# Kernel tuning notes

Hardware: AMD Instinct MI355X
Metric: run time of the kernel (lower is better)

The kernel has to match this reference:

```python
import jax, jax.numpy as jnp
import numpy as np

N = 100000
E = 1600000
F_IN = 32
HID = 16
C_OUT = 10
K = 4


def setup_inputs() -> dict:
    key = jax.random.key(0)
    k1, k2, k3, k4, k5, k6, k7 = jax.random.split(key, 7)
    x = jax.random.normal(k1, (N, F_IN), dtype=jnp.float32)
    edge_index = jax.random.randint(k2, (2, E), 0, N, dtype=jnp.int64)
    # ChebConv weights: one [in, out] matrix per Chebyshev order k
    W1 = jax.random.normal(k3, (K, F_IN, HID), dtype=jnp.float32) / np.sqrt(F_IN)
    b1 = jax.random.normal(k4, (HID,), dtype=jnp.float32) * 0.01
    W2 = jax.random.normal(k5, (K, HID, C_OUT), dtype=jnp.float32) / np.sqrt(HID)
    b2 = jax.random.normal(k6, (C_OUT,), dtype=jnp.float32) * 0.01
    return {"x": x, "edge_index": edge_index, "W1": W1, "b1": b1, "W2": W2, "b2": b2}


def _cheb_conv(h, src, dst, norm, W, b, num_nodes):
    # Tx_0 = h; Tx_1 = L_hat h; Tx_k = 2 L_hat Tx_{k-1} - Tx_{k-2}
    def prop(v):  # v: [N, F] -> L_hat v via sparse gather/scatter
        return jax.ops.segment_sum(norm[:, None] * v[src], dst, num_segments=num_nodes)

    Tx0 = h
    out = Tx0 @ W[0]
    Tx1 = prop(h)
    out = out + Tx1 @ W[1]
    for k in range(2, W.shape[0]):
        Tx2 = 2.0 * prop(Tx1) - Tx0
        out = out + Tx2 @ W[k]
        Tx0, Tx1 = Tx1, Tx2
    return out + b


def reference(x, edge_index, W1, b1, W2, b2):
    src, dst = edge_index[0], edge_index[1]
    num_nodes = x.shape[0]
    # symmetric normalization with lambda_max = 2: L_hat = -D^{-1/2} A D^{-1/2}
    deg = jax.ops.segment_sum(jnp.ones((src.shape[0],), dtype=x.dtype), dst, num_segments=num_nodes)
    dis = jnp.where(deg > 0, jax.lax.rsqrt(jnp.maximum(deg, 1.0)), 0.0)
    norm = -dis[src] * dis[dst]
    h = _cheb_conv(x, src, dst, norm, W1, b1, num_nodes)
    h = jax.nn.relu(h)
    # dropout is identity in eval mode
    h = _cheb_conv(h, src, dst, norm, W2, b2, num_nodes)
    return jax.nn.log_softmax(h, axis=1)
```

## Files before the change

kernel.cpp:

```cpp
#include <hip/hip_runtime.h>
#include <hip/hip_bf16.h>
#include <math.h>


#define BLK 256
#define BLKP 512
#define NBUCK_MAX 256
#define CHUNK 4096
#define CAPB 16384
#define PLACE_CAP 10240

__device__ inline unsigned short f32_to_bf16_rne(float f) {
    unsigned int u = __float_as_uint(f);
    unsigned int rounding = 0x7FFFu + ((u >> 16) & 1u);
    return (unsigned short)((u + rounding) >> 16);
}
__device__ inline unsigned int pack_bf16x2(float a, float b) {
    return (unsigned int)f32_to_bf16_rne(a) | ((unsigned int)f32_to_bf16_rne(b) << 16);
}
__device__ inline void unpack8(const uint4 u, float* f) {
    const unsigned int* p = &u.x;
#pragma unroll
    for (int j = 0; j < 4; j++) {
        unsigned int w = p[j];
        f[2 * j]     = __uint_as_float(w << 16);
        f[2 * j + 1] = __uint_as_float(w & 0xFFFF0000u);
    }
}
__device__ inline void add8(const uint4 u, float* acc) {
    const unsigned int* p = &u.x;
#pragma unroll
    for (int j = 0; j < 4; j++) {
        unsigned int w = p[j];
        acc[2 * j]     += __uint_as_float(w << 16);
        acc[2 * j + 1] += __uint_as_float(w & 0xFFFF0000u);
    }
}
__device__ inline uint4 pack8(const float* r) {
    uint4 o;
    o.x = pack_bf16x2(r[0], r[1]);
    o.y = pack_bf16x2(r[2], r[3]);
    o.z = pack_bf16x2(r[4], r[5]);
    o.w = pack_bf16x2(r[6], r[7]);
    return o;
}

__device__ inline void gather_sum(const int* __restrict__ psrc, int b, int e,
                                  const uint4* __restrict__ vb, int c, float* acc) {
    int i = b;
    for (; i + 7 < e; i += 8) {
        int s0 = psrc[i],     s1 = psrc[i + 1], s2 = psrc[i + 2], s3 = psrc[i + 3];
        int s4 = psrc[i + 4], s5 = psrc[i + 5], s6 = psrc[i + 6], s7 = psrc[i + 7];
        uint4 a0 = vb[(size_t)s0 * 2 + c];
        uint4 a1 = vb[(size_t)s1 * 2 + c];
        uint4 a2 = vb[(size_t)s2 * 2 + c];
        uint4 a3 = vb[(size_t)s3 * 2 + c];
        uint4 a4 = vb[(size_t)s4 * 2 + c];
        uint4 a5 = vb[(size_t)s5 * 2 + c];
        uint4 a6 = vb[(size_t)s6 * 2 + c];
        uint4 a7 = vb[(size_t)s7 * 2 + c];
        add8(a0, acc); add8(a1, acc); add8(a2, acc); add8(a3, acc);
        add8(a4, acc); add8(a5, acc); add8(a6, acc); add8(a7, acc);
    }
    for (; i + 3 < e; i += 4) {
        int s0 = psrc[i], s1 = psrc[i + 1], s2 = psrc[i + 2], s3 = psrc[i + 3];
        uint4 a0 = vb[(size_t)s0 * 2 + c];
        uint4 a1 = vb[(size_t)s1 * 2 + c];
        uint4 a2 = vb[(size_t)s2 * 2 + c];
        uint4 a3 = vb[(size_t)s3 * 2 + c];
        add8(a0, acc); add8(a1, acc); add8(a2, acc); add8(a3, acc);
    }
    for (; i < e; i++) add8(vb[(size_t)psrc[i] * 2 + c], acc);
}

__global__ __launch_bounds__(BLK)
void binned_scatter_kernel(const int* __restrict__ src, const int* __restrict__ dst,
                           int* __restrict__ bfill, int* __restrict__ tmp,
                           int E, int nbuck) {
    __shared__ int cnt[NBUCK_MAX];
    __shared__ int lofs[NBUCK_MAX + 1];
    __shared__ int pos[NBUCK_MAX];
    __shared__ int gbase[NBUCK_MAX];
    __shared__ int stage[CHUNK];
    __shared__ unsigned char bkt[CHUNK];

    int tid = threadIdx.x;
    int e0 = blockIdx.x * CHUNK;
    int nE = min(CHUNK, E - e0);

    for (int b = tid; b < nbuck; b += BLK) { cnt[b] = 0; pos[b] = 0; }
    __syncthreads();

    for (int i = tid; i < nE; i += BLK) {
        int d = dst[e0 + i];
        atomicAdd(&cnt[d >> 9], 1);
    }
    __syncthreads();

    {
        int v = (tid < nbuck) ? cnt[tid] : 0;
        lofs[tid] = v;
        __syncthreads();
        for (int off = 1; off < BLK; off <<= 1) {
            int t = (tid >= off) ? lofs[tid - off] : 0;
            __syncthreads();
            lofs[tid] += t;
            __syncthreads();
        }
        int incl = lofs[tid];
        __syncthreads();
        lofs[tid] = incl - v;
        if (tid == 0) lofs[nbuck] = nE;
        if (tid < nbuck && v > 0)
            gbase[tid] = tid * CAPB + atomicAdd(&bfill[tid], v);
    }
    __syncthreads();

    for (int i = tid; i < nE; i += BLK) {
        int s = src[e0 + i];
        int d = dst[e0 + i];
        int b = d >> 9;
        int slot = lofs[b] + atomicAdd(&pos[b], 1);
        stage[slot] = (s << 9) | (d & 511);
        bkt[slot] = (unsigned char)b;
    }
    __syncthreads();

    for (int i = tid; i < nE; i += BLK) {
        int b = bkt[i];
        tmp[gbase[b] + (i - lofs[b])] = stage[i];
    }
}

__global__ __launch_bounds__(BLKP)
void bucket_place_kernel(const int* __restrict__ bfill, const int* __restrict__ tmp,
                         int* __restrict__ psrc, int2* __restrict__ rows,
                         float* __restrict__ dis, float* __restrict__ d2,
                         float* __restrict__ inv, int N) {
    __shared__ int cnt[512];
    __shared__ int ofs[512];
    __shared__ int fill[512];
    __shared__ int stage[PLACE_CAP];

    int b = blockIdx.x;
    int tid = threadIdx.x;
    int n0 = b << 9;
    int nn = min(512, N - n0);
    int S = b * CAPB;
    int tot = bfill[b];

    cnt[tid] = 0;
    fill[tid] = 0;
    __syncthreads();

    for (int i = tid; i < tot; i += BLKP)
        atomicAdd(&cnt[tmp[S + i] & 511], 1);
    __syncthreads();

    int v = cnt[tid];
    ofs[tid] = v;
    __syncthreads();
    for (int off = 1; off < BLKP; off <<= 1) {
        int t = (tid >= off) ? ofs[tid - off] : 0;
        __syncthreads();
        ofs[tid] += t;
        __syncthreads();
    }
    int excl = ofs[tid] - v;
    __syncthreads();
    ofs[tid] = excl;
    if (tid < nn) {
        int n = n0 + tid;
        rows[n] = make_int2(S + excl, S + excl + v);
        float fv = (float)v;
        dis[n] = (v > 0) ? rsqrtf(fv) : 0.0f;
        d2[n]  = (v > 0) ? 1.0f / fv : 0.0f;
        inv[n] = (v > 0) ? sqrtf(fv) : 0.0f;
    }
    __syncthreads();

    if (tot <= PLACE_CAP) {
        for (int i = tid; i < tot; i += BLKP) {
            int rec = tmp[S + i];
            int nl = rec & 511;
            int slot = ofs[nl] + atomicAdd(&fill[nl], 1);
            stage[slot] = rec >> 9;
        }
        __syncthreads();
        for (int i = tid; i < tot; i += BLKP) psrc[S + i] = stage[i];
    } else {
        for (int i = tid; i < tot; i += BLKP) {
            int rec = tmp[S + i];
            int nl = rec & 511;
            int slot = S + ofs[nl] + atomicAdd(&fill[nl], 1);
            psrc[slot] = rec >> 9;
        }
    }
}


__global__ __launch_bounds__(BLK)
void zgen_kernel(const float* __restrict__ x, const float* __restrict__ dis,
                 const float* __restrict__ W1,
                 uint4* __restrict__ z0t, uint4* __restrict__ uz1t,
                 uint4* __restrict__ uz2t, uint4* __restrict__ uz3t,
                 uint4* __restrict__ z2rt, int N) {
    __shared__ float sW[4 * 32 * 16];
    for (int i = threadIdx.x; i < 4 * 32 * 16; i += blockDim.x) sW[i] = W1[i];
    __syncthreads();
    int t = blockIdx.x * blockDim.x + threadIdx.x;
    int n = t >> 1;
    int h = t & 1;
    if (n >= N) return;
    float acc0[8], acc1[8], acc2[8], acc3[8];
#pragma unroll
    for (int j = 0; j < 8; j++) { acc0[j] = 0.f; acc1[j] = 0.f; acc2[j] = 0.f; acc3[j] = 0.f; }
    const float4* x4 = reinterpret_cast<const float4*>(x + (size_t)n * 32);
#pragma unroll
    for (int q = 0; q < 8; q++) {
        float4 a = x4[q];
        float xi[4] = {a.x, a.y, a.z, a.w};
#pragma unroll
        for (int u = 0; u < 4; u++) {
            const float* Wb = sW + (q * 4 + u) * 16 + h * 8;
            float xv = xi[u];
#pragma unroll
            for (int j = 0; j < 8; j++) {
                acc0[j] += xv * Wb[j];
                acc1[j] += xv * Wb[512 + j];
                acc2[j] += xv * Wb[1024 + j];
                acc3[j] += xv * Wb[1536 + j];
            }
        }
    }
    float dn = dis[n];
    float s1[8], s2[8], s3[8];
#pragma unroll
    for (int j = 0; j < 8; j++) { s1[j] = dn * acc1[j]; s2[j] = dn * acc2[j]; s3[j] = dn * acc3[j]; }
    size_t o = (size_t)n * 2 + h;
    z0t[o]  = pack8(acc0);
    uz1t[o] = pack8(s1);
    uz2t[o] = pack8(s2);
    z2rt[o] = pack8(acc2);
    uz3t[o] = pack8(s3);
}

template <bool HAVE_SUB>
__global__ __launch_bounds__(BLK)
void prop_cl_kernel(const int2* __restrict__ rows,
                    const int* __restrict__ psrc, const float* __restrict__ d2,
                    const uint4* __restrict__ vb, const uint4* __restrict__ addt,
                    const uint4* __restrict__ subt, uint4* __restrict__ outb, int N) {
    int t = blockIdx.x * blockDim.x + threadIdx.x;
    int n = t >> 2;
    int l = t & 3;
    int c = l & 1;
    int hf = l >> 1;
    if (n >= N) return;
    int2 rw = rows[n];
    int beg = rw.x;
    int end = rw.y;
    int mid = beg + ((end - beg) >> 1);
    int b = hf ? mid : beg;
    int e = hf ? end : mid;
    float acc[8];
#pragma unroll
    for (int j = 0; j < 8; j++) acc[j] = 0.f;
    gather_sum(psrc, b, e, vb, c, acc);
#pragma unroll
    for (int j = 0; j < 8; j++) acc[j] += __shfl_xor(acc[j], 2);
    if (hf) return;
    float f = -2.0f * d2[n];
    float ad[8], r[8];
    unpack8(addt[(size_t)n * 2 + c], ad);
    if (HAVE_SUB) {
        float sb[8];
        unpack8(subt[(size_t)n * 2 + c], sb);
#pragma unroll
        for (int j = 0; j < 8; j++) r[j] = f * acc[j] + ad[j] - sb[j];
    } else {
#pragma unroll
        for (int j = 0; j < 8; j++) r[j] = f * acc[j] + ad[j];
    }
    outb[(size_t)n * 2 + c] = pack8(r);
}

__global__ __launch_bounds__(BLK)
void final1_kernel(const int2* __restrict__ rows,
                   const int* __restrict__ psrc, const float* __restrict__ dis,
                   const float* __restrict__ d2, const float* __restrict__ inv,
                   const uint4* __restrict__ ub1t, const uint4* __restrict__ ub2t,
                   const uint4* __restrict__ z0t, const uint4* __restrict__ z2rt,
                   const float* __restrict__ W2, const float* __restrict__ b1,
                   uint4* __restrict__ w0t, uint4* __restrict__ uw1t,
                   uint4* __restrict__ uw2t, uint4* __restrict__ uw3t,
                   uint4* __restrict__ w2rt, int N) {
    __shared__ float sW[4 * 16 * 16];
    __shared__ float sb1[16];
    for (int i = threadIdx.x; i < 4 * 16 * 16; i += blockDim.x) {
        int k = i >> 8, rem = i & 255, j = rem >> 4, o = rem & 15;
        sW[i] = (o < 10) ? W2[k * 160 + j * 10 + o] : 0.0f;
    }
    if (threadIdx.x < 16) sb1[threadIdx.x] = b1[threadIdx.x];
    __syncthreads();
    int t = blockIdx.x * blockDim.x + threadIdx.x;
    int n = t >> 1;
    int h = t & 1;
    if (n >= N) return;
    int2 rw = rows[n];
    float acc[8];
#pragma unroll
    for (int j = 0; j < 8; j++) acc[j] = 0.f;
    gather_sum(psrc, rw.x, rw.y, ub1t, h, acc);
    size_t o2 = (size_t)n * 2 + h;
    float z0[8], hrow[8];
    unpack8(z0t[o2], z0);
    if (d2[n] == 0.0f) {
        float z2[8];
        unpack8(z2rt[o2], z2);
#pragma unroll
        for (int j = 0; j < 8; j++) hrow[j] = fmaxf(sb1[h * 8 + j] + z0[j] - z2[j], 0.0f);
    } else {
        float b2v[8];
        unpack8(ub2t[o2], b2v);
        float dn = dis[n], iv = inv[n];
#pragma unroll
        for (int j = 0; j < 8; j++)
            hrow[j] = fmaxf(sb1[h * 8 + j] + z0[j] - dn * acc[j] - iv * b2v[j], 0.0f);
    }
    float h16[16];
#pragma unroll
    for (int j = 0; j < 8; j++) {
        float other = __shfl_xor(hrow[j], 1);
        h16[h * 8 + j] = hrow[j];
        h16[(1 - h) * 8 + j] = other;
    }
    float w0[8], w1[8], w2[8], w3[8];
#pragma unroll
    for (int o = 0; o < 8; o++) { w0[o] = 0.f; w1[o] = 0.f; w2[o] = 0.f; w3[o] = 0.f; }
#pragma unroll
    for (int j = 0; j < 16; j++) {
        float hv = h16[j];
        const float* Wb = sW + j * 16 + h * 8;
#pragma unroll
        for (int o = 0; o < 8; o++) {
            w0[o] += hv * Wb[o];
            w1[o] += hv * Wb[256 + o];
            w2[o] += hv * Wb[512 + o];
            w3[o] += hv * Wb[768 + o];
        }
    }
    float dn = dis[n];
    float s1[8], s2[8], s3[8];
#pragma unroll
    for (int o = 0; o < 8; o++) { s1[o] = dn * w1[o]; s2[o] = dn * w2[o]; s3[o] = dn * w3[o]; }
    w0t[o2]  = pack8(w0);
    uw1t[o2] = pack8(s1);
    uw2t[o2] = pack8(s2);
    w2rt[o2] = pack8(w2);
    uw3t[o2] = pack8(s3);
}

__global__ __launch_bounds__(BLK)
void final2_kernel(const int2* __restrict__ rows,
                   const int* __restrict__ psrc, const float* __restrict__ dis,
                   const float* __restrict__ d2, const float* __restrict__ inv,
                   const uint4* __restrict__ uv1t, const uint4* __restrict__ uv2t,
                   const uint4* __restrict__ w0t, const uint4* __restrict__ w2rt,
                   const float* __restrict__ b2, float* __restrict__ out, int N) {
    __shared__ float sb2[16];
    if (threadIdx.x < 16) sb2[threadIdx.x] = (threadIdx.x < 10) ? b2[threadIdx.x] : 0.0f;
    __syncthreads();
    int t = blockIdx.x * blockDim.x + threadIdx.x;
    int n = t >> 2;
    int l = t & 3;
    int c = l & 1;
    int hf = l >> 1;
    if (n >= N) return;
    int2 rw = rows[n];
    int beg = rw.x;
    int end = rw.y;
    int mid = beg + ((end - beg) >> 1);
    int gb = hf ? mid : beg;
    int ge = hf ? end : mid;
    float acc[8];
#pragma unroll
    for (int j = 0; j < 8; j++) acc[j] = 0.f;
    gather_sum(psrc, gb, ge, uv1t, c, acc);
#pragma unroll
    for (int j = 0; j < 8; j++) acc[j] += __shfl_xor(acc[j], 2);
    if (hf) return;
    size_t o2 = (size_t)n * 2 + c;
    float w0[8], L[8];
    unpack8(w0t[o2], w0);
    if (d2[n] == 0.0f) {
        float w2[8];
        unpack8(w2rt[o2], w2);
#pragma unroll
        for (int j = 0; j < 8; j++) L[j] = sb2[c * 8 + j] + w0[j] - w2[j];
    } else {
        float v2[8];
        unpack8(uv2t[o2], v2);
        float dn = dis[n], iv = inv[n];
#pragma unroll
        for (int j = 0; j < 8; j++)
            L[j] = sb2[c * 8 + j] + w0[j] - dn * acc[j] - iv * v2[j];
    }
    int nreal = (c == 0) ? 8 : 2;
    float m = -3.0e38f;
    for (int j = 0; j < nreal; j++) m = fmaxf(m, L[j]);
    m = fmaxf(m, __shfl_xor(m, 1));
    float s = 0.0f;
    for (int j = 0; j < nreal; j++) s += expf(L[j] - m);
    s += __shfl_xor(s, 1);
    float lse = m + logf(s);
    float* op = out + (size_t)n * 10 + c * 8;
    for (int j = 0; j < nreal; j++) op[j] = L[j] - lse;
}

extern "C" void kernel_launch(void* const* d_in, const int* in_sizes, int n_in,
                              void* d_out, int out_size, void* d_ws, size_t ws_size,
                              hipStream_t stream) {
    const float* x  = (const float*)d_in[0];
    const int*   ei = (const int*)d_in[1];
    const float* W1 = (const float*)d_in[2];
    const float* b1 = (const float*)d_in[3];
    const float* W2 = (const float*)d_in[4];
    const float* b2 = (const float*)d_in[5];
    float* out = (float*)d_out;

    const int N = in_sizes[0] / 32;
    const int E = in_sizes[1] / 2;
    const int* src = ei;
    const int* dst = ei + E;

    const int nbuck = (N + 511) / 512;

    char* w = (char*)d_ws;
    int*   bfill  = (int*)w;              w += NBUCK_MAX * 4;
    int2*  rows   = (int2*)w;             w += (size_t)(N + 8) * 8;
    float* dis    = (float*)w;            w += (size_t)N * 4;
    float* d2     = (float*)w;            w += (size_t)N * 4;
    float* inv    = (float*)w;            w += (size_t)N * 4;
    int*   tmp    = (int*)w;              w += (size_t)NBUCK_MAX * CAPB * 4;
    int*   psrc   = (int*)w;              w += (size_t)NBUCK_MAX * CAPB * 4;
    uint4* z0t    = (uint4*)w;            w += (size_t)32 * N;
    uint4* uz1t   = (uint4*)w;            w += (size_t)32 * N;
    uint4* uz2t   = (uint4*)w;            w += (size_t)32 * N;
    uint4* uz3t   = (uint4*)w;            w += (size_t)32 * N;
    uint4* z2rt   = (uint4*)w;            w += (size_t)32 * N;
    uint4* ub2t   = (uint4*)w;            w += (size_t)32 * N;
    uint4* ub1t   = (uint4*)w;            w += (size_t)32 * N;
    uint4* w0t    = (uint4*)w;            w += (size_t)32 * N;
    uint4* uw1t   = (uint4*)w;            w += (size_t)32 * N;
    uint4* uw2t   = (uint4*)w;            w += (size_t)32 * N;
    uint4* uw3t   = (uint4*)w;            w += (size_t)32 * N;
    uint4* w2rt   = (uint4*)w;            w += (size_t)32 * N;
    uint4* uv2t   = (uint4*)w;            w += (size_t)32 * N;
    uint4* uv1t   = (uint4*)w;            w += (size_t)32 * N;

    int gN2 = (N * 2 + BLK - 1) / BLK;
    int gN4 = (N * 4 + BLK - 1) / BLK;
    int gCH = (E + CHUNK - 1) / CHUNK;

    hipMemsetAsync(bfill, 0, NBUCK_MAX * sizeof(int), stream);
    binned_scatter_kernel<<<gCH, BLK, 0, stream>>>(src, dst, bfill, tmp, E, nbuck);
    bucket_place_kernel<<<nbuck, BLKP, 0, stream>>>(bfill, tmp, psrc, rows,
                                                    dis, d2, inv, N);

    zgen_kernel<<<gN2, BLK, 0, stream>>>(x, dis, W1, z0t, uz1t, uz2t, uz3t, z2rt, N);
    prop_cl_kernel<false><<<gN4, BLK, 0, stream>>>(rows, psrc, d2,
                                                   uz3t, uz2t, nullptr, ub2t, N);
    prop_cl_kernel<true ><<<gN4, BLK, 0, stream>>>(rows, psrc, d2,
                                                   ub2t, uz1t, uz3t, ub1t, N);
    final1_kernel<<<gN2, BLK, 0, stream>>>(rows, psrc, dis, d2, inv,
                                           ub1t, ub2t, z0t, z2rt, W2, b1,
                                           w0t, uw1t, uw2t, uw3t, w2rt, N);

    prop_cl_kernel<false><<<gN4, BLK, 0, stream>>>(rows, psrc, d2,
                                                   uw3t, uw2t, nullptr, uv2t, N);
    prop_cl_kernel<true ><<<gN4, BLK, 0, stream>>>(rows, psrc, d2,
                                                   uv2t, uw1t, uw3t, uv1t, N);
    final2_kernel<<<gN4, BLK, 0, stream>>>(rows, psrc, dis, d2, inv,
                                           uv1t, uv2t, w0t, w2rt, b2, out, N);
}
```

Measured before the change: 242.8 us.

## Compute node degrees during binning and use wave-shuffle scans in CSR build

The binning kernel now keeps each thread's 16 destination indices in registers and reuses them across passes. It also atomically accumulates per-node degrees into a global array, so the placement kernel no longer re-reads the bucket to count per-node entries. Both block-level prefix scans move from shared-memory Hillis-Steele loops with many barriers to 64-lane wave shuffle scans plus a small cross-wave sum. This trades a second pass over tmp for about 1.6M global atomics on the degree array and a larger memset.

New measurement: 296.3 us. 22.0% more time.

```diff
diff --git a/kernel.cpp b/kernel.cpp
--- a/kernel.cpp
+++ b/kernel.cpp
@@ -7,6 +7,7 @@
 #define BLKP 512
 #define NBUCK_MAX 256
 #define CHUNK 4096
+#define EPT 16
 #define CAPB 16384
 #define PLACE_CAP 10240
 
@@ -75,12 +76,13 @@
 
 __global__ __launch_bounds__(BLK)
 void binned_scatter_kernel(const int* __restrict__ src, const int* __restrict__ dst,
-                           int* __restrict__ bfill, int* __restrict__ tmp,
-                           int E, int nbuck) {
+                           int* __restrict__ bfill, int* __restrict__ deg,
+                           int* __restrict__ tmp, int E, int nbuck) {
     __shared__ int cnt[NBUCK_MAX];
-    __shared__ int lofs[NBUCK_MAX + 1];
+    __shared__ int lofs[NBUCK_MAX];
     __shared__ int pos[NBUCK_MAX];
     __shared__ int gbase[NBUCK_MAX];
+    __shared__ int wsum[4];
     __shared__ int stage[CHUNK];
     __shared__ unsigned char bkt[CHUNK];
 
@@ -91,38 +93,52 @@
     for (int b = tid; b < nbuck; b += BLK) { cnt[b] = 0; pos[b] = 0; }
     __syncthreads();
 
-    for (int i = tid; i < nE; i += BLK) {
-        int d = dst[e0 + i];
-        atomicAdd(&cnt[d >> 9], 1);
+    int myd[EPT];
+#pragma unroll
+    for (int k = 0; k < EPT; k++) {
+        int i = tid + k * BLK;
+        myd[k] = (i < nE) ? dst[e0 + i] : -1;
+    }
+#pragma unroll
+    for (int k = 0; k < EPT; k++) {
+        if (myd[k] >= 0) {
+            atomicAdd(&cnt[myd[k] >> 9], 1);
+            atomicAdd(&deg[myd[k]], 1);
+        }
     }
     __syncthreads();
 
     {
         int v = (tid < nbuck) ? cnt[tid] : 0;
-        lofs[tid] = v;
+        int lane = tid & 63, wv = tid >> 6;
+        int x = v;
+#pragma unroll
+        for (int off = 1; off < 64; off <<= 1) {
+            int y = __shfl_up(x, off);
+            if (lane >= off) x += y;
+        }
+        if (lane == 63) wsum[wv] = x;
         __syncthreads();
-        for (int off = 1; off < BLK; off <<= 1) {
-            int t = (tid >= off) ? lofs[tid - off] : 0;
-            __syncthreads();
-            lofs[tid] += t;
-            __syncthreads();
-        }
-        int incl = lofs[tid];
-        __syncthreads();
-        lofs[tid] = incl - v;
-        if (tid == 0) lofs[nbuck] = nE;
-        if (tid < nbuck && v > 0)
-            gbase[tid] = tid * CAPB + atomicAdd(&bfill[tid], v);
-    }
-    __syncthreads();
-
-    for (int i = tid; i < nE; i += BLK) {
-        int s = src[e0 + i];
-        int d = dst[e0 + i];
-        int b = d >> 9;
-        int slot = lofs[b] + atomicAdd(&pos[b], 1);
-        stage[slot] = (s << 9) | (d & 511);
-        bkt[slot] = (unsigned char)b;
+        int wo = 0;
+        for (int k = 0; k < wv; k++) wo += wsum[k];
+        int excl = x + wo - v;
+        if (tid < nbuck) {
+            lofs[tid] = excl;
+            if (v > 0) gbase[tid] = tid * CAPB + atomicAdd(&bfill[tid], v);
+        }
+    }
+    __syncthreads();
+
+#pragma unroll
+    for (int k = 0; k < EPT; k++) {
+        int i = tid + k * BLK;
+        if (myd[k] >= 0) {
+            int s = src[e0 + i];
+            int b = myd[k] >> 9;
+            int slot = lofs[b] + atomicAdd(&pos[b], 1);
+            stage[slot] = (s << 9) | (myd[k] & 511);
+            bkt[slot] = (unsigned char)b;
+        }
     }
     __syncthreads();
 
@@ -133,13 +149,14 @@
 }
 
 __global__ __launch_bounds__(BLKP)
-void bucket_place_kernel(const int* __restrict__ bfill, const int* __restrict__ tmp,
+void bucket_place_kernel(const int* __restrict__ bfill, const int* __restrict__ deg,
+                         const int* __restrict__ tmp,
                          int* __restrict__ psrc, int2* __restrict__ rows,
                          float* __restrict__ dis, float* __restrict__ d2,
                          float* __restrict__ inv, int N) {
-    __shared__ int cnt[512];
     __shared__ int ofs[512];
     __shared__ int fill[512];
+    __shared__ int wsum[8];
     __shared__ int stage[PLACE_CAP];
 
     int b = blockIdx.x;
@@ -149,25 +166,21 @@
     int S = b * CAPB;
     int tot = bfill[b];
 
-    cnt[tid] = 0;
+    int v = (tid < nn) ? deg[n0 + tid] : 0;
     fill[tid] = 0;
-    __syncthreads();
-
-    for (int i = tid; i < tot; i += BLKP)
-        atomicAdd(&cnt[tmp[S + i] & 511], 1);
-    __syncthreads();
-
-    int v = cnt[tid];
-    ofs[tid] = v;
-    __syncthreads();
-    for (int off = 1; off < BLKP; off <<= 1) {
-        int t = (tid >= off) ? ofs[tid - off] : 0;
-        __syncthreads();
-        ofs[tid] += t;
-        __syncthreads();
-    }
-    int excl = ofs[tid] - v;
-    __syncthreads();
+
+    int lane = tid & 63, wv = tid >> 6;
+    int x = v;
+#pragma unroll
+    for (int off = 1; off < 64; off <<= 1) {
+        int y = __shfl_up(x, off);
+        if (lane >= off) x += y;
+    }
+    if (lane == 63) wsum[wv] = x;
+    __syncthreads();
+    int wo = 0;
+    for (int k = 0; k < wv; k++) wo += wsum[k];
+    int excl = x + wo - v;
     ofs[tid] = excl;
     if (tid < nn) {
         int n = n0 + tid;
@@ -438,6 +451,7 @@
 
     char* w = (char*)d_ws;
     int*   bfill  = (int*)w;              w += NBUCK_MAX * 4;
+    int*   deg    = (int*)w;              w += (size_t)(N + 16) * 4;
     int2*  rows   = (int2*)w;             w += (size_t)(N + 8) * 8;
     float* dis    = (float*)w;            w += (size_t)N * 4;
     float* d2     = (float*)w;            w += (size_t)N * 4;
@@ -463,9 +477,9 @@
     int gN4 = (N * 4 + BLK - 1) / BLK;
     int gCH = (E + CHUNK - 1) / CHUNK;
 
-    hipMemsetAsync(bfill, 0, NBUCK_MAX * sizeof(int), stream);
-    binned_scatter_kernel<<<gCH, BLK, 0, stream>>>(src, dst, bfill, tmp, E, nbuck);
-    bucket_place_kernel<<<nbuck, BLKP, 0, stream>>>(bfill, tmp, psrc, rows,
+    hipMemsetAsync(bfill, 0, (NBUCK_MAX + N + 16) * sizeof(int), stream);
+    binned_scatter_kernel<<<gCH, BLK, 0, stream>>>(src, dst, bfill, deg, tmp, E, nbuck);
+    bucket_place_kernel<<<nbuck, BLKP, 0, stream>>>(bfill, deg, tmp, psrc, rows,
                                                     dis, d2, inv, N);
 
     zgen_kernel<<<gN2, BLK, 0, stream>>>(x, dis, W1, z0t, uz1t, uz2t, uz3t, z2rt, N);
```

## Store layer-2 features as 10-wide split bf16 arrays to cut gather bytes

Applied to the files above, without the earlier changes.

Layer-2 intermediates were padded to 16 bf16 channels (32 bytes per node). They are now split into a 16-byte uint4 array holding channels 0-7 and a 4-byte array holding channels 8-9, so each gathered edge reads 20 bytes instead of 32. A new prop_l2_kernel and the reworked final2_kernel use one thread pair per node covering all 10 channels, with the edge list split in half and reduced by a shuffle. The log-softmax no longer needs a cross-lane reduction. The cost is two separate loads per edge, one of them a narrow 4-byte scattered load, and fewer threads per node.

New measurement: 249.9 us. 1.03x slower.

```diff
diff --git a/kernel.cpp b/kernel.cpp
--- a/kernel.cpp
+++ b/kernel.cpp
@@ -27,6 +27,10 @@
         f[2 * j + 1] = __uint_as_float(w & 0xFFFF0000u);
     }
 }
+__device__ inline void unpack2(unsigned int w, float* f) {
+    f[0] = __uint_as_float(w << 16);
+    f[1] = __uint_as_float(w & 0xFFFF0000u);
+}
 __device__ inline void add8(const uint4 u, float* acc) {
     const unsigned int* p = &u.x;
 #pragma unroll
@@ -35,6 +39,10 @@
         acc[2 * j]     += __uint_as_float(w << 16);
         acc[2 * j + 1] += __uint_as_float(w & 0xFFFF0000u);
     }
+}
+__device__ inline void add2(unsigned int w, float* acc) {
+    acc[0] += __uint_as_float(w << 16);
+    acc[1] += __uint_as_float(w & 0xFFFF0000u);
 }
 __device__ inline uint4 pack8(const float* r) {
     uint4 o;
@@ -71,6 +79,36 @@
         add8(a0, acc); add8(a1, acc); add8(a2, acc); add8(a3, acc);
     }
     for (; i < e; i++) add8(vb[(size_t)psrc[i] * 2 + c], acc);
+}
+
+__device__ inline void gather_sum10(const int* __restrict__ psrc, int b, int e,
+                                    const uint4* __restrict__ vA,
+                                    const unsigned int* __restrict__ vB, float* acc) {
+    int i = b;
+    for (; i + 7 < e; i += 8) {
+        int s0 = psrc[i],     s1 = psrc[i + 1], s2 = psrc[i + 2], s3 = psrc[i + 3];
+        int s4 = psrc[i + 4], s5 = psrc[i + 5], s6 = psrc[i + 6], s7 = psrc[i + 7];
+        uint4 a0 = vA[s0], a1 = vA[s1], a2 = vA[s2], a3 = vA[s3];
+        uint4 a4 = vA[s4], a5 = vA[s5], a6 = vA[s6], a7 = vA[s7];
+        unsigned int q0 = vB[s0], q1 = vB[s1], q2 = vB[s2], q3 = vB[s3];
+        unsigned int q4 = vB[s4], q5 = vB[s5], q6 = vB[s6], q7 = vB[s7];
+        add8(a0, acc); add8(a1, acc); add8(a2, acc); add8(a3, acc);
+        add8(a4, acc); add8(a5, acc); add8(a6, acc); add8(a7, acc);
+        add2(q0, acc + 8); add2(q1, acc + 8); add2(q2, acc + 8); add2(q3, acc + 8);
+        add2(q4, acc + 8); add2(q5, acc + 8); add2(q6, acc + 8); add2(q7, acc + 8);
+    }
+    for (; i + 3 < e; i += 4) {
+        int s0 = psrc[i], s1 = psrc[i + 1], s2 = psrc[i + 2], s3 = psrc[i + 3];
+        uint4 a0 = vA[s0], a1 = vA[s1], a2 = vA[s2], a3 = vA[s3];
+        unsigned int q0 = vB[s0], q1 = vB[s1], q2 = vB[s2], q3 = vB[s3];
+        add8(a0, acc); add8(a1, acc); add8(a2, acc); add8(a3, acc);
+        add2(q0, acc + 8); add2(q1, acc + 8); add2(q2, acc + 8); add2(q3, acc + 8);
+    }
+    for (; i < e; i++) {
+        int s = psrc[i];
+        add8(vA[s], acc);
+        add2(vB[s], acc + 8);
+    }
 }
 
 __global__ __launch_bounds__(BLK)
@@ -292,9 +330,11 @@
                    const uint4* __restrict__ ub1t, const uint4* __restrict__ ub2t,
                    const uint4* __restrict__ z0t, const uint4* __restrict__ z2rt,
                    const float* __restrict__ W2, const float* __restrict__ b1,
-                   uint4* __restrict__ w0t, uint4* __restrict__ uw1t,
-                   uint4* __restrict__ uw2t, uint4* __restrict__ uw3t,
-                   uint4* __restrict__ w2rt, int N) {
+                   uint4* __restrict__ w0A, unsigned int* __restrict__ w0B,
+                   uint4* __restrict__ uw1A, unsigned int* __restrict__ uw1B,
+                   uint4* __restrict__ uw2A, unsigned int* __restrict__ uw2B,
+                   uint4* __restrict__ uw3A, unsigned int* __restrict__ uw3B,
+                   uint4* __restrict__ w2rA, unsigned int* __restrict__ w2rB, int N) {
     __shared__ float sW[4 * 16 * 16];
     __shared__ float sb1[16];
     for (int i = threadIdx.x; i < 4 * 16 * 16; i += blockDim.x) {
@@ -354,28 +394,79 @@
     float s1[8], s2[8], s3[8];
 #pragma unroll
     for (int o = 0; o < 8; o++) { s1[o] = dn * w1[o]; s2[o] = dn * w2[o]; s3[o] = dn * w3[o]; }
-    w0t[o2]  = pack8(w0);
-    uw1t[o2] = pack8(s1);
-    uw2t[o2] = pack8(s2);
-    w2rt[o2] = pack8(w2);
-    uw3t[o2] = pack8(s3);
+    if (h == 0) {
+        w0A[n]  = pack8(w0);
+        uw1A[n] = pack8(s1);
+        uw2A[n] = pack8(s2);
+        w2rA[n] = pack8(w2);
+        uw3A[n] = pack8(s3);
+    } else {
+        w0B[n]  = pack_bf16x2(w0[0], w0[1]);
+        uw1B[n] = pack_bf16x2(s1[0], s1[1]);
+        uw2B[n] = pack_bf16x2(s2[0], s2[1]);
+        w2rB[n] = pack_bf16x2(w2[0], w2[1]);
+        uw3B[n] = pack_bf16x2(s3[0], s3[1]);
+    }
+}
+
+template <bool HAVE_SUB>
+__global__ __launch_bounds__(BLK)
+void prop_l2_kernel(const int2* __restrict__ rows,
+                    const int* __restrict__ psrc, const float* __restrict__ d2,
+                    const uint4* __restrict__ vA, const unsigned int* __restrict__ vB,
+                    const uint4* __restrict__ addA, const unsigned int* __restrict__ addB,
+                    const uint4* __restrict__ subA, const unsigned int* __restrict__ subB,
+                    uint4* __restrict__ outA, unsigned int* __restrict__ outB, int N) {
+    int t = blockIdx.x * blockDim.x + threadIdx.x;
+    int n = t >> 1;
+    int hf = t & 1;
+    if (n >= N) return;
+    int2 rw = rows[n];
+    int beg = rw.x;
+    int end = rw.y;
+    int mid = beg + ((end - beg) >> 1);
+    int b = hf ? mid : beg;
+    int e = hf ? end : mid;
+    float acc[10];
+#pragma unroll
+    for (int j = 0; j < 10; j++) acc[j] = 0.f;
+    gather_sum10(psrc, b, e, vA, vB, acc);
+#pragma unroll
+    for (int j = 0; j < 10; j++) acc[j] += __shfl_xor(acc[j], 1);
+    if (hf) return;
+    float f = -2.0f * d2[n];
+    float ad[10], r[10];
+    unpack8(addA[n], ad);
+    unpack2(addB[n], ad + 8);
+    if (HAVE_SUB) {
+        float sb[10];
+        unpack8(subA[n], sb);
+        unpack2(subB[n], sb + 8);
+#pragma unroll
+        for (int j = 0; j < 10; j++) r[j] = f * acc[j] + ad[j] - sb[j];
+    } else {
+#pragma unroll
+        for (int j = 0; j < 10; j++) r[j] = f * acc[j] + ad[j];
+    }
+    outA[n] = pack8(r);
+    outB[n] = pack_bf16x2(r[8], r[9]);
 }
 
 __global__ __launch_bounds__(BLK)
 void final2_kernel(const int2* __restrict__ rows,
                    const int* __restrict__ psrc, const float* __restrict__ dis,
                    const float* __restrict__ d2, const float* __restrict__ inv,
-                   const uint4* __restrict__ uv1t, const uint4* __restrict__ uv2t,
-                   const uint4* __restrict__ w0t, const uint4* __restrict__ w2rt,
+                   const uint4* __restrict__ uv1A, const unsigned int* __restrict__ uv1B,
+                   const uint4* __restrict__ uv2A, const unsigned int* __restrict__ uv2B,
+                   const uint4* __restrict__ w0A, const unsigned int* __restrict__ w0B,
+                   const uint4* __restrict__ w2rA, const unsigned int* __restrict__ w2rB,
                    const float* __restrict__ b2, float* __restrict__ out, int N) {
     __shared__ float sb2[16];
     if (threadIdx.x < 16) sb2[threadIdx.x] = (threadIdx.x < 10) ? b2[threadIdx.x] : 0.0f;
     __syncthreads();
     int t = blockIdx.x * blockDim.x + threadIdx.x;
-    int n = t >> 2;
-    int l = t & 3;
-    int c = l & 1;
-    int hf = l >> 1;
+    int n = t >> 1;
+    int hf = t & 1;
     if (n >= N) return;
     int2 rw = rows[n];
     int beg = rw.x;
@@ -383,39 +474,41 @@
     int mid = beg + ((end - beg) >> 1);
     int gb = hf ? mid : beg;
     int ge = hf ? end : mid;
-    float acc[8];
-#pragma unroll
-    for (int j = 0; j < 8; j++) acc[j] = 0.f;
-    gather_sum(psrc, gb, ge, uv1t, c, acc);
-#pragma unroll
-    for (int j = 0; j < 8; j++) acc[j] += __shfl_xor(acc[j], 2);
+    float acc[10];
+#pragma unroll
+    for (int j = 0; j < 10; j++) acc[j] = 0.f;
+    gather_sum10(psrc, gb, ge, uv1A, uv1B, acc);
+#pragma unroll
+    for (int j = 0; j < 10; j++) acc[j] += __shfl_xor(acc[j], 1);
     if (hf) return;
-    size_t o2 = (size_t)n * 2 + c;
-    float w0[8], L[8];
-    unpack8(w0t[o2], w0);
+    float w0[10], L[10];
+    unpack8(w0A[n], w0);
+    unpack2(w0B[n], w0 + 8);
     if (d2[n] == 0.0f) {
-        float w2[8];
-        unpack8(w2rt[o2], w2);
-#pragma unroll
-        for (int j = 0; j < 8; j++) L[j] = sb2[c * 8 + j] + w0[j] - w2[j];
+        float w2[10];
+        unpack8(w2rA[n], w2);
+        unpack2(w2rB[n], w2 + 8);
+#pragma unroll
+        for (int j = 0; j < 10; j++) L[j] = sb2[j] + w0[j] - w2[j];
     } else {
-        float v2[8];
-        unpack8(uv2t[o2], v2);
+        float v2[10];
+        unpack8(uv2A[n], v2);
+        unpack2(uv2B[n], v2 + 8);
         float dn = dis[n], iv = inv[n];
 #pragma unroll
-        for (int j = 0; j < 8; j++)
-            L[j] = sb2[c * 8 + j] + w0[j] - dn * acc[j] - iv * v2[j];
-    }
-    int nreal = (c == 0) ? 8 : 2;
-    float m = -3.0e38f;
-    for (int j = 0; j < nreal; j++) m = fmaxf(m, L[j]);
-    m = fmaxf(m, __shfl_xor(m, 1));
+        for (int j = 0; j < 10; j++)
+            L[j] = sb2[j] + w0[j] - dn * acc[j] - iv * v2[j];
+    }
+    float m = L[0];
+#pragma unroll
+    for (int j = 1; j < 10; j++) m = fmaxf(m, L[j]);
     float s = 0.0f;
-    for (int j = 0; j < nreal; j++) s += expf(L[j] - m);
-    s += __shfl_xor(s, 1);
+#pragma unroll
+    for (int j = 0; j < 10; j++) s += expf(L[j] - m);
     float lse = m + logf(s);
-    float* op = out + (size_t)n * 10 + c * 8;
-    for (int j = 0; j < nreal; j++) op[j] = L[j] - lse;
+    float* op = out + (size_t)n * 10;
+#pragma unroll
+    for (int j = 0; j < 10; j++) op[j] = L[j] - lse;
 }
 
 extern "C" void kernel_launch(void* const* d_in, const int* in_sizes, int n_in,
@@ -451,13 +544,20 @@
     uint4* z2rt   = (uint4*)w;            w += (size_t)32 * N;
     uint4* ub2t   = (uint4*)w;            w += (size_t)32 * N;
     uint4* ub1t   = (uint4*)w;            w += (size_t)32 * N;
-    uint4* w0t    = (uint4*)w;            w += (size_t)32 * N;
-    uint4* uw1t   = (uint4*)w;            w += (size_t)32 * N;
-    uint4* uw2t   = (uint4*)w;            w += (size_t)32 * N;
-    uint4* uw3t   = (uint4*)w;            w += (size_t)32 * N;
-    uint4* w2rt   = (uint4*)w;            w += (size_t)32 * N;
-    uint4* uv2t   = (uint4*)w;            w += (size_t)32 * N;
-    uint4* uv1t   = (uint4*)w;            w += (size_t)32 * N;
+    uint4* w0A    = (uint4*)w;            w += (size_t)16 * N;
+    uint4* uw1A   = (uint4*)w;            w += (size_t)16 * N;
+    uint4* uw2A   = (uint4*)w;            w += (size_t)16 * N;
+    uint4* uw3A   = (uint4*)w;            w += (size_t)16 * N;
+    uint4* w2rA   = (uint4*)w;            w += (size_t)16 * N;
+    uint4* uv2A   = (uint4*)w;            w += (size_t)16 * N;
+    uint4* uv1A   = (uint4*)w;            w += (size_t)16 * N;
+    unsigned int* w0B  = (unsigned int*)w; w += (size_t)4 * N;
+    unsigned int* uw1B = (unsigned int*)w; w += (size_t)4 * N;
+    unsigned int* uw2B = (unsigned int*)w; w += (size_t)4 * N;
+    unsigned int* uw3B = (unsigned int*)w; w += (size_t)4 * N;
+    unsigned int* w2rB = (unsigned int*)w; w += (size_t)4 * N;
+    unsigned int* uv2B = (unsigned int*)w; w += (size_t)4 * N;
+    unsigned int* uv1B = (unsigned int*)w; w += (size_t)4 * N;
 
     int gN2 = (N * 2 + BLK - 1) / BLK;
     int gN4 = (N * 4 + BLK - 1) / BLK;
@@ -475,12 +575,16 @@
                                                    ub2t, uz1t, uz3t, ub1t, N);
     final1_kernel<<<gN2, BLK, 0, stream>>>(rows, psrc, dis, d2, inv,
                                            ub1t, ub2t, z0t, z2rt, W2, b1,
-                                           w0t, uw1t, uw2t, uw3t, w2rt, N);
-
-    prop_cl_kernel<false><<<gN4, BLK, 0, stream>>>(rows, psrc, d2,
-                                                   uw3t, uw2t, nullptr, uv2t, N);
-    prop_cl_kernel<true ><<<gN4, BLK, 0, stream>>>(rows, psrc, d2,
-                                                   uv2t, uw1t, uw3t, uv1t, N);
-    final2_kernel<<<gN4, BLK, 0, stream>>>(rows, psrc, dis, d2, inv,
-                                           uv1t, uv2t, w0t, w2rt, b2, out, N);
-}
+                                           w0A, w0B, uw1A, uw1B, uw2A, uw2B,
+                                           uw3A, uw3B, w2rA, w2rB, N);
+
+    prop_l2_kernel<false><<<gN2, BLK, 0, stream>>>(rows, psrc, d2,
+                                                   uw3A, uw3B, uw2A, uw2B,
+                                                   nullptr, nullptr, uv2A, uv2B, N);
+    prop_l2_kernel<true ><<<gN2, BLK, 0, stream>>>(rows, psrc, d2,
+                                                   uv2A, uv2B, uw1A, uw1B,
+                                                   uw3A, uw3B, uv1A, uv1B, N);
+    final2_kernel<<<gN2, BLK, 0, stream>>>(rows, psrc, dis, d2, inv,
+                                           uv1A, uv1B, uv2A, uv2B,
+                                           w0A, w0B, w2rA, w2rB, b2, out, N);
+}
```
